# Kernel optimization log

Hardware: AMD Instinct MI355X
Metric: run time of the kernel (lower is better)

Reference implementation:

```python
import jax, jax.numpy as jnp
import numpy as np

N, S, D = 2, 2048, 512
HEADS, HEAD_DIM = 8, 64
SCALE_BASE = 512.0
EPS = 1e-08


def xpos_apply(x, positions, downscale):
    # x: (B, S, d)  positions: (B, S) float
    d = x.shape[-1]
    half = jnp.arange(0, d, 2, dtype=jnp.float32)
    scale_vec = (half + 0.4 * d) / (1.4 * d)                      # (d/2,)
    power = positions[..., None] / SCALE_BASE                     # (B, S, 1)
    scale = scale_vec ** power                                    # (B, S, d/2)
    inv_freq = 1.0 / (10000.0 ** (half / d))                      # (d/2,)
    sinusoid = positions[..., None] * inv_freq                    # (B, S, d/2)
    sin = jnp.sin(sinusoid)
    cos = jnp.cos(sinusoid)
    if downscale:
        scale = 1.0 / scale
    # duplicate-interleave to full dim
    sin = jnp.repeat(sin, 2, axis=-1)
    cos = jnp.repeat(cos, 2, axis=-1)
    scale = jnp.repeat(scale, 2, axis=-1)
    x1 = x[..., 0::2]
    x2 = x[..., 1::2]
    rot = jnp.stack([-x2, x1], axis=-1).reshape(x.shape)          # rotate_every_two
    return (x * cos + rot * sin) * scale


def split_heads(x):
    # (N, S, H*Hd) -> (N*H, S, Hd)
    return x.reshape(N, S, HEADS, HEAD_DIM).transpose(0, 2, 1, 3).reshape(N * HEADS, S, HEAD_DIM)


def setup_inputs() -> dict:
    key = jax.random.key(0)
    ks = jax.random.split(key, 8)
    g = 1.0 / np.sqrt(D)
    return {
        'sequence': jax.random.normal(ks[0], (N, S, D), dtype=jnp.float32),
        'input_mask': jnp.ones((N, S), dtype=jnp.float32),
        'positions': jnp.tile(jnp.arange(S, dtype=jnp.int32), (N, 1)),
        'layer_num': 0,
        'Wq': jax.random.normal(ks[1], (D, D), dtype=jnp.float32) * g,
        'bq': jnp.zeros((D,), dtype=jnp.float32),
        'Wk': jax.random.normal(ks[2], (D, D), dtype=jnp.float32) * g,
        'bk': jnp.zeros((D,), dtype=jnp.float32),
        'Wv': jax.random.normal(ks[3], (D, D), dtype=jnp.float32) * g,
        'bv': jnp.zeros((D,), dtype=jnp.float32),
        'Wo': jax.random.normal(ks[4], (D, D), dtype=jnp.float32) * g,
        'bo': jnp.zeros((D,), dtype=jnp.float32),
    }


def reference(sequence, input_mask, positions, layer_num, Wq, bq, Wk, bk, Wv, bv, Wo, bo):
    scaling = HEAD_DIM ** (-0.5)
    posf = positions.astype(jnp.float32)

    Q = split_heads(sequence @ Wq.T + bq) * scaling               # (N*H, S, Hd)
    K = split_heads(sequence @ Wk.T + bk)
    V = split_heads(sequence @ Wv.T + bv)

    pos_h = jnp.repeat(posf, HEADS, axis=0)                       # 'n s -> (n h) s'
    K = xpos_apply(K, pos_h, downscale=True)
    Q = xpos_apply(Q, pos_h, downscale=False)

    A = jnp.einsum('nsd,ntd->nst', Q, K).reshape(N, HEADS, S, S)  # (N, H, S, S2)
    Vh = V.reshape(N, HEADS, S, HEAD_DIM)

    # causal mask: input_mask over kv dim, lower-triangular
    tri = jnp.tril(jnp.ones((S, S), dtype=jnp.float32))
    attn_mask = input_mask[:, None, None, :] * tri[None, None]    # (N, 1, S, S2)

    A = jax.nn.sigmoid(A) * attn_mask

    # stick-breaking decay: reverse-cumprod of (1 - A) along kv dim, shifted
    Af = jnp.flip(A, axis=(2, 3))
    C = jnp.exp(jnp.cumsum(jnp.log(1.0 - Af + EPS), axis=-1))
    C = jnp.flip(C, axis=(2, 3))
    C = jnp.concatenate([jnp.ones((N, HEADS, S, 1), dtype=C.dtype), C[..., :-1]], axis=-1)

    A = C * A
    attended = jnp.einsum('nhst,nhtd->nhsd', A, Vh)               # (N, H, S, Hd)
    attended = attended.transpose(0, 2, 1, 3).reshape(N, S, HEADS * HEAD_DIM)
    out = attended @ Wo.T + bo
    return out
```

## Files before the change

kernel.cpp:

```cpp
#include <hip/hip_runtime.h>
#include <math.h>

#define S_LEN 2048
#define DMODEL 512
#define HDIM 64
#define EPS_G 1e-8f

typedef __bf16 bf16x8 __attribute__((ext_vector_type(8)));
typedef __bf16 bf16x4 __attribute__((ext_vector_type(4)));
typedef float f32x4 __attribute__((ext_vector_type(4)));

template <int CTRL>
__device__ __forceinline__ float dpp_mov(float src, float oldv) {
  return __int_as_float(__builtin_amdgcn_update_dpp(
      __float_as_int(oldv), __float_as_int(src), CTRL, 0xF, 0xF, false));
}
#define ROW_SHL(n) (0x100 + (n))
#define ROW_SHR(n) (0x110 + (n))

__device__ __forceinline__ float swz_head(float v) {
  return __int_as_float(__builtin_amdgcn_ds_swizzle(__float_as_int(v), 0x0010));
}
__device__ __forceinline__ float swz_tail(float v) {
  return __int_as_float(__builtin_amdgcn_ds_swizzle(__float_as_int(v), 0x01F0));
}

__global__ __launch_bounds__(256) void cvt_kernel(
    const float* __restrict__ X, const float* __restrict__ Wq,
    const float* __restrict__ Wk, const float* __restrict__ Wv,
    const float* __restrict__ Wo,
    __bf16* __restrict__ Xb, __bf16* __restrict__ Wb, __bf16* __restrict__ Wob) {
  const int u = blockIdx.x * 256 + threadIdx.x;
  const float* src; __bf16* dst; int off;
  if (u < 524288)      { src = X;  dst = Xb;          off = u; }
  else if (u < 589824) { src = Wq; dst = Wb;          off = u - 524288; }
  else if (u < 655360) { src = Wk; dst = Wb + 262144; off = u - 589824; }
  else if (u < 720896) { src = Wv; dst = Wb + 524288; off = u - 655360; }
  else                 { src = Wo; dst = Wob;         off = u - 720896; }
  const float4 v = *(const float4*)(src + (size_t)off * 4);
  bf16x4 o;
  o[0] = (__bf16)v.x; o[1] = (__bf16)v.y; o[2] = (__bf16)v.z; o[3] = (__bf16)v.w;
  *(bf16x4*)(dst + (size_t)off * 4) = o;
}

__global__ __launch_bounds__(256, 2) void qkv_gemm(
    const __bf16* __restrict__ Xb, const __bf16* __restrict__ Wb,
    const float* __restrict__ bq, const float* __restrict__ bk, const float* __restrict__ bv,
    const int* __restrict__ pos,
    __bf16* __restrict__ Qh, __bf16* __restrict__ Kh, __bf16* __restrict__ Vt) {
  const int i0 = blockIdx.x << 6;
  const int h  = blockIdx.y;
  const int j0 = h << 6;

  __shared__ __bf16 Xs[64][72];
  __shared__ __bf16 Wls[3][64][72];

  const int tid = threadIdx.x;
  const int wv = tid >> 6, lane = tid & 63;
  const int l = lane & 15, seg = lane >> 4;
  const int sr = tid >> 2, sc = (tid & 3) << 4;

  f32x4 O[3][4];
#pragma unroll
  for (int w = 0; w < 3; ++w)
#pragma unroll
    for (int nt = 0; nt < 4; ++nt) O[w][nt] = (f32x4){0.f, 0.f, 0.f, 0.f};

  bf16x8 xr0, xr1, wr[3][2];
#define LOADQKV(K0)                                                                   \
  {                                                                                   \
    const __bf16* xp = Xb + (size_t)(i0 + sr) * 512 + (K0) + sc;                      \
    xr0 = *(const bf16x8*)xp; xr1 = *(const bf16x8*)(xp + 8);                         \
    _Pragma("unroll")                                                                 \
    for (int w = 0; w < 3; ++w) {                                                     \
      const __bf16* wp = Wb + (size_t)w * 262144 + (size_t)(j0 + sr) * 512 + (K0) + sc;\
      wr[w][0] = *(const bf16x8*)wp; wr[w][1] = *(const bf16x8*)(wp + 8);             \
    }                                                                                 \
  }

  LOADQKV(0)
  for (int k0 = 0; k0 < 512; k0 += 64) {
    __syncthreads();
    *(bf16x8*)&Xs[sr][sc]     = xr0;
    *(bf16x8*)&Xs[sr][sc + 8] = xr1;
#pragma unroll
    for (int w = 0; w < 3; ++w) {
      *(bf16x8*)&Wls[w][sr][sc]     = wr[w][0];
      *(bf16x8*)&Wls[w][sr][sc + 8] = wr[w][1];
    }
    __syncthreads();
    if (k0 < 448) LOADQKV(k0 + 64)

    bf16x8 a0 = *(const bf16x8*)&Xs[wv * 16 + l][seg * 8];
    bf16x8 a1 = *(const bf16x8*)&Xs[wv * 16 + l][seg * 8 + 32];
#pragma unroll
    for (int w = 0; w < 3; ++w)
#pragma unroll
      for (int nt = 0; nt < 4; ++nt) {
        bf16x8 b0 = *(const bf16x8*)&Wls[w][nt * 16 + l][seg * 8];
        bf16x8 b1 = *(const bf16x8*)&Wls[w][nt * 16 + l][seg * 8 + 32];
        O[w][nt] = __builtin_amdgcn_mfma_f32_16x16x32_bf16(a0, b0, O[w][nt], 0, 0, 0);
        O[w][nt] = __builtin_amdgcn_mfma_f32_16x16x32_bf16(a1, b1, O[w][nt], 0, 0, 0);
      }
  }

  const float* const bsrc[3] = {bq, bk, bv};
#pragma unroll
  for (int w = 0; w < 3; ++w)
#pragma unroll
    for (int nt = 0; nt < 4; ++nt) {
      const float bb = bsrc[w][j0 + nt * 16 + l];
#pragma unroll
      for (int reg = 0; reg < 4; ++reg) O[w][nt][reg] += bb;
    }

  const int n = i0 >> 11, sb = i0 & 2047;
  const int nh = (n << 3) + h;
  const int sl = wv * 16 + seg * 4;

  float invf[4], l2sv[4];
#pragma unroll
  for (int nt = 0; nt < 4; ++nt) {
    const float kp = (float)((nt * 16 + l) >> 1);
    invf[nt] = exp2f(-0.41524100f * kp);
    l2sv[nt] = log2f((2.f * kp + 25.6f) * (1.f / 89.6f));
  }
  float pv_[4];
#pragma unroll
  for (int reg = 0; reg < 4; ++reg)
    pv_[reg] = (float)pos[n * S_LEN + sb + sl + reg];

  __syncthreads();

#pragma unroll
  for (int w = 0; w < 2; ++w) {
    const float qs  = (w == 0) ? 0.125f : 1.f;
    const float sgn = (w == 0) ? 1.f : -1.f;
    __bf16* __restrict__ Ob = (w == 0) ? Qh : Kh;
#pragma unroll
    for (int reg = 0; reg < 4; ++reg) {
      const float p = pv_[reg];
#pragma unroll
      for (int nt = 0; nt < 4; ++nt) {
        const float x  = O[w][nt][reg];
        const float xp = __shfl_xor(x, 1);
        const float ang = p * invf[nt];
        const float sn = sinf(ang), cn = cosf(ang);
        const float scl = exp2f(sgn * p * (1.f / 512.f) * l2sv[nt]) * qs;
        const int d = nt * 16 + l;
        const float o = (d & 1) ? (x * cn + xp * sn) : (x * cn - xp * sn);
        Xs[sl + reg][d] = (__bf16)(o * scl);
      }
    }
    __syncthreads();
    __bf16* dst = Ob + (((size_t)nh * S_LEN + sb + sr) << 6) + sc;
    *(bf16x8*)dst       = *(bf16x8*)&Xs[sr][sc];
    *(bf16x8*)(dst + 8) = *(bf16x8*)&Xs[sr][sc + 8];
    __syncthreads();
  }

#pragma unroll
  for (int reg = 0; reg < 4; ++reg)
#pragma unroll
    for (int nt = 0; nt < 4; ++nt)
      Xs[sl + reg][nt * 16 + l] = (__bf16)O[2][nt][reg];
  __syncthreads();
  const int d = tid >> 2, part = tid & 3;
  __bf16 tmp[16];
#pragma unroll
  for (int i = 0; i < 16; ++i) tmp[i] = Xs[part * 16 + i][d];
  __bf16* dst = Vt + (((size_t)(nh * 64 + d)) << 11) + sb + part * 16;
  *(bf16x8*)dst       = *(bf16x8*)&tmp[0];
  *(bf16x8*)(dst + 8) = *(bf16x8*)&tmp[8];
}

__global__ __launch_bounds__(256, 2) void attn_chunk(
    const __bf16* __restrict__ Qh, const __bf16* __restrict__ Kh,
    const __bf16* __restrict__ Vt, const float* __restrict__ imask,
    __bf16* __restrict__ att, float* __restrict__ PartO,
    float* __restrict__ PartP, float* __restrict__ PartA0) {
  const int id = blockIdx.x;
  const int nh = id & 15;
  const int t  = id >> 4;
  int rb, c, nc;
  if (t < 8)       { rb = t; c = 0; nc = 1; }
  else if (t < 24) { int u = t - 8;  rb = 8  + (u >> 1); c = u & 1;     nc = 2; }
  else if (t < 48) { int u = t - 24; rb = 16 + u / 3;    c = u - 3 * (u / 3); nc = 3; }
  else             { int u = t - 48; rb = 24 + (u >> 2); c = u & 3;     nc = 4; }
  const int hi = rb - (c << 3);
  const int lo = (c == nc - 1) ? 0 : hi - 7;

  const int n = nh >> 3, h = nh & 7;
  const int tid = threadIdx.x;
  const int wv = tid >> 6, lane = tid & 63;
  const int l = lane & 15, seg = lane >> 4;
  const int pr = tid >> 3, pc = (tid & 7) << 3;

  __shared__ __bf16 Qs16[64][72];
  __shared__ __bf16 Ks16[64][72];
  __shared__ __bf16 Vt16[64][72];
  __shared__ __bf16 cs16[64][72];
  __shared__ float msk[64];

  for (int idx = tid; idx < 512; idx += 256) {
    int r = idx >> 3, c8 = (idx & 7) << 3;
    *(bf16x8*)&Qs16[r][c8] =
        *(const bf16x8*)(Qh + (((size_t)nh * S_LEN + rb * 64 + r) << 6) + c8);
  }

  f32x4 O[4];
  float pend[4][4];
  float Crow[4];
  float a0k0[4];
#pragma unroll
  for (int nt = 0; nt < 4; ++nt) O[nt] = (f32x4){0.f, 0.f, 0.f, 0.f};
#pragma unroll
  for (int r = 0; r < 4; ++r) {
    Crow[r] = 1.f; a0k0[r] = 0.f;
#pragma unroll
    for (int nt = 0; nt < 4; ++nt) pend[r][nt] = 0.f;
  }

  bf16x8 kp0, kp1, vp0, vp1;
  float mp = 0.f;
#define LOADKV(JT)                                                                     \
  kp0 = *(const bf16x8*)(Kh + (((size_t)nh * S_LEN + (JT) * 64 + pr) << 6) + pc);      \
  kp1 = *(const bf16x8*)(Kh + (((size_t)nh * S_LEN + (JT) * 64 + 32 + pr) << 6) + pc); \
  vp0 = *(const bf16x8*)(Vt + (((size_t)(nh * 64 + pr)) << 11) + (JT) * 64 + pc);      \
  vp1 = *(const bf16x8*)(Vt + (((size_t)(nh * 64 + 32 + pr)) << 11) + (JT) * 64 + pc); \
  if (tid < 64) mp = imask[n * S_LEN + (JT) * 64 + tid];

  LOADKV(hi)

  for (int jt = hi; jt >= lo; --jt) {
    __syncthreads();
    *(bf16x8*)&Ks16[pr][pc]      = kp0;
    *(bf16x8*)&Ks16[32 + pr][pc] = kp1;
    *(bf16x8*)&Vt16[pr][pc]      = vp0;
    *(bf16x8*)&Vt16[32 + pr][pc] = vp1;
    if (tid < 64) msk[tid] = mp;
    __syncthreads();
    if (jt > lo) { LOADKV(jt - 1) }

    bf16x8 aq0 = *(const bf16x8*)&Qs16[wv * 16 + l][seg * 8];
    bf16x8 aq1 = *(const bf16x8*)&Qs16[wv * 16 + l][seg * 8 + 32];
    f32x4 Sv[4];
#pragma unroll
    for (int nt = 0; nt < 4; ++nt) {
      bf16x8 bk0 = *(const bf16x8*)&Ks16[nt * 16 + l][seg * 8];
      bf16x8 bk1 = *(const bf16x8*)&Ks16[nt * 16 + l][seg * 8 + 32];
      f32x4 z = (f32x4){0.f, 0.f, 0.f, 0.f};
      z = __builtin_amdgcn_mfma_f32_16x16x32_bf16(aq0, bk0, z, 0, 0, 0);
      z = __builtin_amdgcn_mfma_f32_16x16x32_bf16(aq1, bk1, z, 0, 0, 0);
      Sv[nt] = z;
    }

    float v0f[4];
#pragma unroll
    for (int nt = 0; nt < 4; ++nt) v0f[nt] = (float)Vt16[nt * 16 + l][0];

#pragma unroll
    for (int reg = 0; reg < 4; ++reg) {
      const int qrow = rb * 64 + wv * 16 + seg * 4 + reg;
      float a_[4], f_[4], p_[4];
#pragma unroll
      for (int nt = 0; nt < 4; ++nt) {
        const int key = jt * 64 + nt * 16 + l;
        const float s = Sv[nt][reg];
        const float mv = msk[nt * 16 + l];
        const float av = (key <= qrow)
            ? mv * __builtin_amdgcn_rcpf(1.f + __expf(-s))
            : 0.f;
        a_[nt] = av;
        f_[nt] = 1.f - av + EPS_G;
      }
#pragma unroll
      for (int nt = 0; nt < 4; ++nt) {
        float p = f_[nt];
        p *= dpp_mov<ROW_SHL(1)>(p, 1.f);
        p *= dpp_mov<ROW_SHL(2)>(p, 1.f);
        p *= dpp_mov<ROW_SHL(4)>(p, 1.f);
        p *= dpp_mov<ROW_SHL(8)>(p, 1.f);
        p_[nt] = p;
      }
      float P_[4], tl[4];
#pragma unroll
      for (int nt = 0; nt < 4; ++nt) {
        P_[nt] = swz_head(p_[nt]);
        tl[nt] = swz_tail(f_[nt]);
      }
      const float a0 = swz_head(a_[0]);
      const float T3 = 1.f, T2 = P_[3], T1 = T2 * P_[2], T0 = T1 * P_[1];
      const float Tarr[4] = {T0, T1, T2, T3};
      const float Ptile = T0 * P_[0];
      const float crow = Crow[reg];
#pragma unroll
      for (int nt = 0; nt < 4; ++nt) {
        const float pprev = dpp_mov<ROW_SHR(1)>(p_[nt], 0.f);
        float cv;
        if (l > 0)
          cv = a_[nt] * pprev * Tarr[nt] * crow;
        else if (nt > 0)
          cv = a_[nt] * tl[nt - 1] * P_[nt] * Tarr[nt] * crow;
        else
          cv = (jt == 0 && nc == 1) ? a_[0] : 0.f;
        cs16[wv * 16 + seg * 4 + reg][nt * 16 + l] = (__bf16)cv;
      }
      if (jt == 0) a0k0[reg] = a0;
      const float f63 = tl[3];
      const float s0  = a0 * Ptile * crow;
      Crow[reg] = crow * Ptile;
#pragma unroll
      for (int nt = 0; nt < 4; ++nt) {
        O[nt][reg] += pend[reg][nt] * f63;
        pend[reg][nt] = s0 * v0f[nt];
      }
    }

    bf16x8 ac0 = *(const bf16x8*)&cs16[wv * 16 + l][seg * 8];
    bf16x8 ac1 = *(const bf16x8*)&cs16[wv * 16 + l][seg * 8 + 32];
#pragma unroll
    for (int nt = 0; nt < 4; ++nt) {
      bf16x8 bv0 = *(const bf16x8*)&Vt16[nt * 16 + l][seg * 8];
      bf16x8 bv1 = *(const bf16x8*)&Vt16[nt * 16 + l][seg * 8 + 32];
      O[nt] = __builtin_amdgcn_mfma_f32_16x16x32_bf16(ac0, bv0, O[nt], 0, 0, 0);
      O[nt] = __builtin_amdgcn_mfma_f32_16x16x32_bf16(ac1, bv1, O[nt], 0, 0, 0);
    }
  }

  if (lo > 0) {
    const int m = lo << 6;
    const float mb = imask[n * S_LEN + m - 1];
    const __bf16* kb = Kh + (((size_t)nh * S_LEN + m - 1) << 6) + seg * 16;
    bf16x8 kb0 = *(const bf16x8*)kb, kb1 = *(const bf16x8*)(kb + 8);
    bf16x8 q0 = *(const bf16x8*)&Qs16[wv * 16 + l][seg * 16];
    bf16x8 q1 = *(const bf16x8*)&Qs16[wv * 16 + l][seg * 16 + 8];
    float sc_ = 0.f;
#pragma unroll
    for (int j = 0; j < 8; ++j)
      sc_ += (float)q0[j] * (float)kb0[j] + (float)q1[j] * (float)kb1[j];
    sc_ += __shfl_xor(sc_, 16);
    sc_ += __shfl_xor(sc_, 32);
    const float fbl = 1.f - mb * __builtin_amdgcn_rcpf(1.f + __expf(-sc_)) + EPS_G;
#pragma unroll
    for (int reg = 0; reg < 4; ++reg) {
      const float fb = __shfl(fbl, (wv << 6 & 0) + (seg << 2) + reg);
#pragma unroll
      for (int nt = 0; nt < 4; ++nt) O[nt][reg] += pend[reg][nt] * fb;
    }
  }

  if (nc == 1) {
#pragma unroll
    for (int nt = 0; nt < 4; ++nt)
#pragma unroll
      for (int reg = 0; reg < 4; ++reg) {
        const int srow = rb * 64 + wv * 16 + seg * 4 + reg;
        att[((size_t)(n * S_LEN + srow)) * DMODEL + h * HDIM + nt * 16 + l] =
            (__bf16)O[nt][reg];
      }
  } else {
    const int slot = nh * 72 + (t - 8);
    float* po = PartO + (size_t)slot * 4096;
#pragma unroll
    for (int nt = 0; nt < 4; ++nt)
#pragma unroll
      for (int reg = 0; reg < 4; ++reg)
        po[(wv * 16 + seg * 4 + reg) * 64 + nt * 16 + l] = O[nt][reg];
    if (l == 0) {
#pragma unroll
      for (int reg = 0; reg < 4; ++reg)
        PartP[slot * 64 + wv * 16 + seg * 4 + reg] = Crow[reg];
      if (lo == 0) {
#pragma unroll
        for (int reg = 0; reg < 4; ++reg)
          PartA0[(nh * 24 + rb - 8) * 64 + wv * 16 + seg * 4 + reg] = a0k0[reg];
      }
    }
  }
}

__global__ __launch_bounds__(256) void combine_kernel(
    const float* __restrict__ PartO, const float* __restrict__ PartP,
    const float* __restrict__ PartA0, const __bf16* __restrict__ Vt,
    __bf16* __restrict__ att) {
  const int b = blockIdx.x;
  const int nh = b / 24;
  const int rb = 8 + (b - nh * 24);
  const int nc = (rb < 16) ? 2 : ((rb < 24) ? 3 : 4);
  const int t0 = (rb < 16) ? 8 + ((rb - 8) << 1)
               : (rb < 24) ? 24 + (rb - 16) * 3
                           : 48 + ((rb - 24) << 2);
  const int n = nh >> 3, h = nh & 7;
  const int tid = threadIdx.x;
  const int r = tid >> 2, db = (tid & 3) << 4;

  float acc[16];
#pragma unroll
  for (int j = 0; j < 16; ++j) acc[j] = 0.f;
  float fac = 1.f;
  for (int c = 0; c < nc; ++c) {
    const int slot = nh * 72 + (t0 - 8) + c;
    const float* po = PartO + (size_t)slot * 4096 + r * 64 + db;
    const float P = PartP[slot * 64 + r];
#pragma unroll
    for (int q = 0; q < 4; ++q) {
      const float4 v = *(const float4*)(po + q * 4);
      acc[q * 4 + 0] += fac * v.x; acc[q * 4 + 1] += fac * v.y;
      acc[q * 4 + 2] += fac * v.z; acc[q * 4 + 3] += fac * v.w;
    }
    fac *= P;
  }
  const float a0 = PartA0[(nh * 24 + rb - 8) * 64 + r];
#pragma unroll
  for (int j = 0; j < 16; ++j)
    acc[j] += a0 * (float)Vt[(((size_t)(nh * 64 + db + j)) << 11)];

  __bf16 ob[16];
#pragma unroll
  for (int j = 0; j < 16; ++j) ob[j] = (__bf16)acc[j];
  __bf16* dst = att + ((size_t)(n * S_LEN + rb * 64 + r)) * DMODEL + h * HDIM + db;
  *(bf16x8*)dst       = *(bf16x8*)&ob[0];
  *(bf16x8*)(dst + 8) = *(bf16x8*)&ob[8];
}

__global__ __launch_bounds__(256, 2) void out_gemm(const __bf16* __restrict__ Xa,
                                                   const __bf16* __restrict__ Wob,
                                                   const float* __restrict__ bo,
                                                   float* __restrict__ Out) {
  const int i0 = blockIdx.x << 6, j0 = blockIdx.y << 7;
  __shared__ __bf16 As[64][72];
  __shared__ __bf16 Bs[128][72];

  const int tid = threadIdx.x;
  const int wv = tid >> 6, lane = tid & 63;
  const int l = lane & 15, seg = lane >> 4;
  const int sr = tid >> 2, sc = (tid & 3) << 4;

  f32x4 O[8];
#pragma unroll
  for (int nt = 0; nt < 8; ++nt) O[nt] = (f32x4){0.f, 0.f, 0.f, 0.f};

  bf16x8 ar0, ar1, br[2][2];
#define LOADOUT(K0)                                                          \
  {                                                                          \
    const __bf16* xp = Xa + (size_t)(i0 + sr) * 512 + (K0) + sc;             \
    ar0 = *(const bf16x8*)xp; ar1 = *(const bf16x8*)(xp + 8);                \
    _Pragma("unroll")                                                        \
    for (int ps = 0; ps < 2; ++ps) {                                         \
      const __bf16* wp = Wob + (size_t)(j0 + ps * 64 + sr) * 512 + (K0) + sc;\
      br[ps][0] = *(const bf16x8*)wp; br[ps][1] = *(const bf16x8*)(wp + 8);  \
    }                                                                        \
  }

  LOADOUT(0)
  for (int k0 = 0; k0 < 512; k0 += 64) {
    __syncthreads();
    *(bf16x8*)&As[sr][sc]     = ar0;
    *(bf16x8*)&As[sr][sc + 8] = ar1;
#pragma unroll
    for (int ps = 0; ps < 2; ++ps) {
      *(bf16x8*)&Bs[ps * 64 + sr][sc]     = br[ps][0];
      *(bf16x8*)&Bs[ps * 64 + sr][sc + 8] = br[ps][1];
    }
    __syncthreads();
    if (k0 < 448) LOADOUT(k0 + 64)

    bf16x8 a0 = *(const bf16x8*)&As[wv * 16 + l][seg * 8];
    bf16x8 a1 = *(const bf16x8*)&As[wv * 16 + l][seg * 8 + 32];
#pragma unroll
    for (int nt = 0; nt < 8; ++nt) {
      bf16x8 b0 = *(const bf16x8*)&Bs[nt * 16 + l][seg * 8];
      bf16x8 b1 = *(const bf16x8*)&Bs[nt * 16 + l][seg * 8 + 32];
      O[nt] = __builtin_amdgcn_mfma_f32_16x16x32_bf16(a0, b0, O[nt], 0, 0, 0);
      O[nt] = __builtin_amdgcn_mfma_f32_16x16x32_bf16(a1, b1, O[nt], 0, 0, 0);
    }
  }

#pragma unroll
  for (int nt = 0; nt < 8; ++nt) {
    const float bb = bo[j0 + nt * 16 + l];
#pragma unroll
    for (int reg = 0; reg < 4; ++reg) {
      const int m = wv * 16 + seg * 4 + reg;
      Out[(size_t)(i0 + m) * 512 + j0 + nt * 16 + l] = O[nt][reg] + bb;
    }
  }
}

extern "C" void kernel_launch(void* const* d_in, const int* in_sizes, int n_in,
                              void* d_out, int out_size, void* d_ws, size_t ws_size,
                              hipStream_t stream) {
  (void)in_sizes; (void)n_in; (void)out_size; (void)ws_size;
  const float* seq  = (const float*)d_in[0];
  const float* mask = (const float*)d_in[1];
  const int*   pos  = (const int*)d_in[2];
  const float* Wq = (const float*)d_in[4];
  const float* bq = (const float*)d_in[5];
  const float* Wk = (const float*)d_in[6];
  const float* bk = (const float*)d_in[7];
  const float* Wv = (const float*)d_in[8];
  const float* bv = (const float*)d_in[9];
  const float* Wo = (const float*)d_in[10];
  const float* bo = (const float*)d_in[11];
  float* out = (float*)d_out;

  char* base = (char*)d_ws;
  __bf16* att = (__bf16*)base;
  __bf16* Qh  = (__bf16*)(base + ( 4u << 20));
  __bf16* Kh  = (__bf16*)(base + ( 8u << 20));
  __bf16* Vt  = (__bf16*)(base + (12u << 20));
  __bf16* Wb  = (__bf16*)(base + (16u << 20));
  __bf16* Wob = (__bf16*)(base + (18u << 20));
  __bf16* Xb  = (__bf16*)(base + (19u << 20));
  float* PartO  = (float*)(base + (23u << 20));
  float* PartP  = (float*)(base + (42u << 20));
  float* PartA0 = (float*)(base + (43u << 20));

  cvt_kernel<<<3072, 256, 0, stream>>>(seq, Wq, Wk, Wv, Wo, Xb, Wb, Wob);
  qkv_gemm<<<dim3(64, 8), 256, 0, stream>>>(Xb, Wb, bq, bk, bv, pos, Qh, Kh, Vt);
  attn_chunk<<<1280, 256, 0, stream>>>(Qh, Kh, Vt, mask, att, PartO, PartP, PartA0);
  combine_kernel<<<384, 256, 0, stream>>>(PartO, PartP, PartA0, Vt, att);
  out_gemm<<<dim3(64, 4), 256, 0, stream>>>(att, Wob, bo, out);
}
```

Measured before the change: 174.6 us.

## Use 128-row query tiles with 512-thread attention blocks and fuse xpos epilogue

The attention chunk kernel now handles 128 query rows per block with 8 waves, so each K/V tile loaded into shared memory serves twice as many queries. Block count halves, scheduling is reversed so heavy blocks launch first, and the combine kernel is remapped to match. The QKV epilogue computes sin/cos and scale once per element for both Q and K using hardware sin/cos on a revolution-normalized angle and a reciprocal, then writes Q, K and V after a single barrier. The risks are lower occupancy and coarser load balance from the larger blocks, plus precision changes from the hardware trig and reciprocal.

```diff
diff --git a/kernel.cpp b/kernel.cpp
--- a/kernel.cpp
+++ b/kernel.cpp
@@ -122,7 +122,7 @@
 #pragma unroll
   for (int nt = 0; nt < 4; ++nt) {
     const float kp = (float)((nt * 16 + l) >> 1);
-    invf[nt] = exp2f(-0.41524100f * kp);
+    invf[nt] = exp2f(-0.41524100f * kp) * 0.15915494f;
     l2sv[nt] = log2f((2.f * kp + 25.6f) * (1.f / 89.6f));
   }
   float pv_[4];
@@ -133,61 +133,62 @@
   __syncthreads();
 
 #pragma unroll
-  for (int w = 0; w < 2; ++w) {
-    const float qs  = (w == 0) ? 0.125f : 1.f;
-    const float sgn = (w == 0) ? 1.f : -1.f;
-    __bf16* __restrict__ Ob = (w == 0) ? Qh : Kh;
-#pragma unroll
-    for (int reg = 0; reg < 4; ++reg) {
-      const float p = pv_[reg];
-#pragma unroll
-      for (int nt = 0; nt < 4; ++nt) {
-        const float x  = O[w][nt][reg];
-        const float xp = __shfl_xor(x, 1);
-        const float ang = p * invf[nt];
-        const float sn = sinf(ang), cn = cosf(ang);
-        const float scl = exp2f(sgn * p * (1.f / 512.f) * l2sv[nt]) * qs;
-        const int d = nt * 16 + l;
-        const float o = (d & 1) ? (x * cn + xp * sn) : (x * cn - xp * sn);
-        Xs[sl + reg][d] = (__bf16)(o * scl);
-      }
-    }
-    __syncthreads();
-    __bf16* dst = Ob + (((size_t)nh * S_LEN + sb + sr) << 6) + sc;
-    *(bf16x8*)dst       = *(bf16x8*)&Xs[sr][sc];
-    *(bf16x8*)(dst + 8) = *(bf16x8*)&Xs[sr][sc + 8];
-    __syncthreads();
-  }
-
-#pragma unroll
-  for (int reg = 0; reg < 4; ++reg)
-#pragma unroll
-    for (int nt = 0; nt < 4; ++nt)
-      Xs[sl + reg][nt * 16 + l] = (__bf16)O[2][nt][reg];
+  for (int reg = 0; reg < 4; ++reg) {
+    const float p = pv_[reg];
+#pragma unroll
+    for (int nt = 0; nt < 4; ++nt) {
+      const int d = nt * 16 + l;
+      const float rev0 = p * invf[nt];
+      const float rev  = rev0 - floorf(rev0);
+      const float sn = __builtin_amdgcn_sinf(rev);
+      const float cn = __builtin_amdgcn_cosf(rev);
+      const float e  = p * (1.f / 512.f) * l2sv[nt];
+      const float sq = exp2f(e);
+      const float sQ = sq * 0.125f;
+      const float sK = __builtin_amdgcn_rcpf(sq);
+      float x  = O[0][nt][reg];
+      float xp = __shfl_xor(x, 1);
+      Xs[sl + reg][d] =
+          (__bf16)((((d & 1) ? (x * cn + xp * sn) : (x * cn - xp * sn))) * sQ);
+      x  = O[1][nt][reg];
+      xp = __shfl_xor(x, 1);
+      Wls[0][sl + reg][d] =
+          (__bf16)((((d & 1) ? (x * cn + xp * sn) : (x * cn - xp * sn))) * sK);
+      Wls[1][sl + reg][d] = (__bf16)O[2][nt][reg];
+    }
+  }
   __syncthreads();
+
+  __bf16* qdst = Qh + (((size_t)nh * S_LEN + sb + sr) << 6) + sc;
+  *(bf16x8*)qdst       = *(bf16x8*)&Xs[sr][sc];
+  *(bf16x8*)(qdst + 8) = *(bf16x8*)&Xs[sr][sc + 8];
+  __bf16* kdst = Kh + (((size_t)nh * S_LEN + sb + sr) << 6) + sc;
+  *(bf16x8*)kdst       = *(bf16x8*)&Wls[0][sr][sc];
+  *(bf16x8*)(kdst + 8) = *(bf16x8*)&Wls[0][sr][sc + 8];
+
   const int d = tid >> 2, part = tid & 3;
   __bf16 tmp[16];
 #pragma unroll
-  for (int i = 0; i < 16; ++i) tmp[i] = Xs[part * 16 + i][d];
-  __bf16* dst = Vt + (((size_t)(nh * 64 + d)) << 11) + sb + part * 16;
-  *(bf16x8*)dst       = *(bf16x8*)&tmp[0];
-  *(bf16x8*)(dst + 8) = *(bf16x8*)&tmp[8];
-}
-
-__global__ __launch_bounds__(256, 2) void attn_chunk(
+  for (int i = 0; i < 16; ++i) tmp[i] = Wls[1][part * 16 + i][d];
+  __bf16* vdst = Vt + (((size_t)(nh * 64 + d)) << 11) + sb + part * 16;
+  *(bf16x8*)vdst       = *(bf16x8*)&tmp[0];
+  *(bf16x8*)(vdst + 8) = *(bf16x8*)&tmp[8];
+}
+
+__global__ __launch_bounds__(512, 4) void attn_chunk(
     const __bf16* __restrict__ Qh, const __bf16* __restrict__ Kh,
     const __bf16* __restrict__ Vt, const float* __restrict__ imask,
     __bf16* __restrict__ att, float* __restrict__ PartO,
     float* __restrict__ PartP, float* __restrict__ PartA0) {
-  const int id = blockIdx.x;
+  const int id = 639 - blockIdx.x;
   const int nh = id & 15;
   const int t  = id >> 4;
-  int rb, c, nc;
-  if (t < 8)       { rb = t; c = 0; nc = 1; }
-  else if (t < 24) { int u = t - 8;  rb = 8  + (u >> 1); c = u & 1;     nc = 2; }
-  else if (t < 48) { int u = t - 24; rb = 16 + u / 3;    c = u - 3 * (u / 3); nc = 3; }
-  else             { int u = t - 48; rb = 24 + (u >> 2); c = u & 3;     nc = 4; }
-  const int hi = rb - (c << 3);
+  int rb2, c, nc;
+  if (t < 4)       { rb2 = t; c = 0; nc = 1; }
+  else if (t < 12) { int u = t - 4;  rb2 = 4  + (u >> 1); c = u & 1; nc = 2; }
+  else if (t < 24) { int u = t - 12; rb2 = 8  + u / 3;    c = u - 3 * (u / 3); nc = 3; }
+  else             { int u = t - 24; rb2 = 12 + (u >> 2); c = u & 3; nc = 4; }
+  const int hi = 2 * rb2 + 1 - (c << 3);
   const int lo = (c == nc - 1) ? 0 : hi - 7;
 
   const int n = nh >> 3, h = nh & 7;
@@ -196,16 +197,16 @@
   const int l = lane & 15, seg = lane >> 4;
   const int pr = tid >> 3, pc = (tid & 7) << 3;
 
-  __shared__ __bf16 Qs16[64][72];
+  __shared__ __bf16 Qs16[128][72];
   __shared__ __bf16 Ks16[64][72];
   __shared__ __bf16 Vt16[64][72];
-  __shared__ __bf16 cs16[64][72];
+  __shared__ __bf16 cs16[128][72];
   __shared__ float msk[64];
 
-  for (int idx = tid; idx < 512; idx += 256) {
+  for (int idx = tid; idx < 1024; idx += 512) {
     int r = idx >> 3, c8 = (idx & 7) << 3;
     *(bf16x8*)&Qs16[r][c8] =
-        *(const bf16x8*)(Qh + (((size_t)nh * S_LEN + rb * 64 + r) << 6) + c8);
+        *(const bf16x8*)(Qh + (((size_t)nh * S_LEN + rb2 * 128 + r) << 6) + c8);
   }
 
   f32x4 O[4];
@@ -221,23 +222,19 @@
     for (int nt = 0; nt < 4; ++nt) pend[r][nt] = 0.f;
   }
 
-  bf16x8 kp0, kp1, vp0, vp1;
+  bf16x8 kp0, vp0;
   float mp = 0.f;
-#define LOADKV(JT)                                                                     \
-  kp0 = *(const bf16x8*)(Kh + (((size_t)nh * S_LEN + (JT) * 64 + pr) << 6) + pc);      \
-  kp1 = *(const bf16x8*)(Kh + (((size_t)nh * S_LEN + (JT) * 64 + 32 + pr) << 6) + pc); \
-  vp0 = *(const bf16x8*)(Vt + (((size_t)(nh * 64 + pr)) << 11) + (JT) * 64 + pc);      \
-  vp1 = *(const bf16x8*)(Vt + (((size_t)(nh * 64 + 32 + pr)) << 11) + (JT) * 64 + pc); \
+#define LOADKV(JT)                                                                  \
+  kp0 = *(const bf16x8*)(Kh + (((size_t)nh * S_LEN + (JT) * 64 + pr) << 6) + pc);   \
+  vp0 = *(const bf16x8*)(Vt + (((size_t)(nh * 64 + pr)) << 11) + (JT) * 64 + pc);   \
   if (tid < 64) mp = imask[n * S_LEN + (JT) * 64 + tid];
 
   LOADKV(hi)
 
   for (int jt = hi; jt >= lo; --jt) {
     __syncthreads();
-    *(bf16x8*)&Ks16[pr][pc]      = kp0;
-    *(bf16x8*)&Ks16[32 + pr][pc] = kp1;
-    *(bf16x8*)&Vt16[pr][pc]      = vp0;
-    *(bf16x8*)&Vt16[32 + pr][pc] = vp1;
+    *(bf16x8*)&Ks16[pr][pc] = kp0;
+    *(bf16x8*)&Vt16[pr][pc] = vp0;
     if (tid < 64) msk[tid] = mp;
     __syncthreads();
     if (jt > lo) { LOADKV(jt - 1) }
@@ -261,7 +258,7 @@
 
 #pragma unroll
     for (int reg = 0; reg < 4; ++reg) {
-      const int qrow = rb * 64 + wv * 16 + seg * 4 + reg;
+      const int qrow = rb2 * 128 + wv * 16 + seg * 4 + reg;
       float a_[4], f_[4], p_[4];
 #pragma unroll
       for (int nt = 0; nt < 4; ++nt) {
@@ -344,7 +341,7 @@
     const float fbl = 1.f - mb * __builtin_amdgcn_rcpf(1.f + __expf(-sc_)) + EPS_G;
 #pragma unroll
     for (int reg = 0; reg < 4; ++reg) {
-      const float fb = __shfl(fbl, (wv << 6 & 0) + (seg << 2) + reg);
+      const float fb = __shfl(fbl, (seg << 2) + reg);
 #pragma unroll
       for (int nt = 0; nt < 4; ++nt) O[nt][reg] += pend[reg][nt] * fb;
     }
@@ -355,13 +352,13 @@
     for (int nt = 0; nt < 4; ++nt)
 #pragma unroll
       for (int reg = 0; reg < 4; ++reg) {
-        const int srow = rb * 64 + wv * 16 + seg * 4 + reg;
+        const int srow = rb2 * 128 + wv * 16 + seg * 4 + reg;
         att[((size_t)(n * S_LEN + srow)) * DMODEL + h * HDIM + nt * 16 + l] =
             (__bf16)O[nt][reg];
       }
   } else {
-    const int slot = nh * 72 + (t - 8);
-    float* po = PartO + (size_t)slot * 4096;
+    const int slot = nh * 36 + (t - 4);
+    float* po = PartO + (size_t)slot * 8192;
 #pragma unroll
     for (int nt = 0; nt < 4; ++nt)
 #pragma unroll
@@ -370,11 +367,11 @@
     if (l == 0) {
 #pragma unroll
       for (int reg = 0; reg < 4; ++reg)
-        PartP[slot * 64 + wv * 16 + seg * 4 + reg] = Crow[reg];
+        PartP[slot * 128 + wv * 16 + seg * 4 + reg] = Crow[reg];
       if (lo == 0) {
 #pragma unroll
         for (int reg = 0; reg < 4; ++reg)
-          PartA0[(nh * 24 + rb - 8) * 64 + wv * 16 + seg * 4 + reg] = a0k0[reg];
+          PartA0[(nh * 12 + rb2 - 4) * 128 + wv * 16 + seg * 4 + reg] = a0k0[reg];
       }
     }
   }
@@ -385,43 +382,45 @@
     const float* __restrict__ PartA0, const __bf16* __restrict__ Vt,
     __bf16* __restrict__ att) {
   const int b = blockIdx.x;
-  const int nh = b / 24;
-  const int rb = 8 + (b - nh * 24);
-  const int nc = (rb < 16) ? 2 : ((rb < 24) ? 3 : 4);
-  const int t0 = (rb < 16) ? 8 + ((rb - 8) << 1)
-               : (rb < 24) ? 24 + (rb - 16) * 3
-                           : 48 + ((rb - 24) << 2);
+  const int nh = b / 12;
+  const int rb2 = 4 + (b - nh * 12);
+  const int nc = (rb2 < 8) ? 2 : ((rb2 < 12) ? 3 : 4);
+  const int t0 = (rb2 < 8) ? 4 + ((rb2 - 4) << 1)
+               : (rb2 < 12) ? 12 + (rb2 - 8) * 3
+                            : 24 + ((rb2 - 12) << 2);
   const int n = nh >> 3, h = nh & 7;
   const int tid = threadIdx.x;
-  const int r = tid >> 2, db = (tid & 3) << 4;
-
-  float acc[16];
-#pragma unroll
-  for (int j = 0; j < 16; ++j) acc[j] = 0.f;
+  const int r = tid >> 1, db = (tid & 1) << 5;
+
+  float acc[32];
+#pragma unroll
+  for (int j = 0; j < 32; ++j) acc[j] = 0.f;
   float fac = 1.f;
   for (int c = 0; c < nc; ++c) {
-    const int slot = nh * 72 + (t0 - 8) + c;
-    const float* po = PartO + (size_t)slot * 4096 + r * 64 + db;
-    const float P = PartP[slot * 64 + r];
-#pragma unroll
-    for (int q = 0; q < 4; ++q) {
+    const int slot = nh * 36 + (t0 - 4) + c;
+    const float* po = PartO + (size_t)slot * 8192 + r * 64 + db;
+    const float P = PartP[slot * 128 + r];
+#pragma unroll
+    for (int q = 0; q < 8; ++q) {
       const float4 v = *(const float4*)(po + q * 4);
       acc[q * 4 + 0] += fac * v.x; acc[q * 4 + 1] += fac * v.y;
       acc[q * 4 + 2] += fac * v.z; acc[q * 4 + 3] += fac * v.w;
     }
     fac *= P;
   }
-  const float a0 = PartA0[(nh * 24 + rb - 8) * 64 + r];
-#pragma unroll
-  for (int j = 0; j < 16; ++j)
+  const float a0 = PartA0[(nh * 12 + rb2 - 4) * 128 + r];
+#pragma unroll
+  for (int j = 0; j < 32; ++j)
     acc[j] += a0 * (float)Vt[(((size_t)(nh * 64 + db + j)) << 11)];
 
-  __bf16 ob[16];
-#pragma unroll
-  for (int j = 0; j < 16; ++j) ob[j] = (__bf16)acc[j];
-  __bf16* dst = att + ((size_t)(n * S_LEN + rb * 64 + r)) * DMODEL + h * HDIM + db;
-  *(bf16x8*)dst       = *(bf16x8*)&ob[0];
-  *(bf16x8*)(dst + 8) = *(bf16x8*)&ob[8];
+  __bf16 ob[32];
+#pragma unroll
+  for (int j = 0; j < 32; ++j) ob[j] = (__bf16)acc[j];
+  __bf16* dst = att + ((size_t)(n * S_LEN + rb2 * 128 + r)) * DMODEL + h * HDIM + db;
+  *(bf16x8*)dst        = *(bf16x8*)&ob[0];
+  *(bf16x8*)(dst + 8)  = *(bf16x8*)&ob[8];
+  *(bf16x8*)(dst + 16) = *(bf16x8*)&ob[16];
+  *(bf16x8*)(dst + 24) = *(bf16x8*)&ob[24];
 }
 
 __global__ __launch_bounds__(256, 2) void out_gemm(const __bf16* __restrict__ Xa,
@@ -519,7 +518,7 @@
 
   cvt_kernel<<<3072, 256, 0, stream>>>(seq, Wq, Wk, Wv, Wo, Xb, Wb, Wob);
   qkv_gemm<<<dim3(64, 8), 256, 0, stream>>>(Xb, Wb, bq, bk, bv, pos, Qh, Kh, Vt);
-  attn_chunk<<<1280, 256, 0, stream>>>(Qh, Kh, Vt, mask, att, PartO, PartP, PartA0);
-  combine_kernel<<<384, 256, 0, stream>>>(PartO, PartP, PartA0, Vt, att);
+  attn_chunk<<<640, 512, 0, stream>>>(Qh, Kh, Vt, mask, att, PartO, PartP, PartA0);
+  combine_kernel<<<192, 256, 0, stream>>>(PartO, PartP, PartA0, Vt, att);
   out_gemm<<<dim3(64, 4), 256, 0, stream>>>(att, Wob, bo, out);
 }
```

Result: no change. 176.4 us (+1.0%).

## Reassign GEMM warp tiles by output column and hoist xPos trig per column

Applied to the files above, without the earlier changes.

In the QKV and output projection kernels, each wave now owns a 16-column slice of the output across all 64 rows instead of a 16-row slice across all columns. As a result, the per-column xPos frequency, scale and bias are computed once per thread instead of once per column tile. The rotary path uses hardware sin/cos on a range-reduced revolution count and a reciprocal for the K downscale, so one exp2 serves both Q and K. Q, K and V are staged into separate shared buffers with a single barrier instead of three sequential store phases, which cuts barriers and transcendental work at some cost to trig precision.

```diff
diff --git a/kernel.cpp b/kernel.cpp
--- a/kernel.cpp
+++ b/kernel.cpp
@@ -64,7 +64,7 @@
 #pragma unroll
   for (int w = 0; w < 3; ++w)
 #pragma unroll
-    for (int nt = 0; nt < 4; ++nt) O[w][nt] = (f32x4){0.f, 0.f, 0.f, 0.f};
+    for (int r4 = 0; r4 < 4; ++r4) O[w][r4] = (f32x4){0.f, 0.f, 0.f, 0.f};
 
   bf16x8 xr0, xr1, wr[3][2];
 #define LOADQKV(K0)                                                                   \
@@ -91,87 +91,85 @@
     __syncthreads();
     if (k0 < 448) LOADQKV(k0 + 64)
 
-    bf16x8 a0 = *(const bf16x8*)&Xs[wv * 16 + l][seg * 8];
-    bf16x8 a1 = *(const bf16x8*)&Xs[wv * 16 + l][seg * 8 + 32];
-#pragma unroll
-    for (int w = 0; w < 3; ++w)
-#pragma unroll
-      for (int nt = 0; nt < 4; ++nt) {
-        bf16x8 b0 = *(const bf16x8*)&Wls[w][nt * 16 + l][seg * 8];
-        bf16x8 b1 = *(const bf16x8*)&Wls[w][nt * 16 + l][seg * 8 + 32];
-        O[w][nt] = __builtin_amdgcn_mfma_f32_16x16x32_bf16(a0, b0, O[w][nt], 0, 0, 0);
-        O[w][nt] = __builtin_amdgcn_mfma_f32_16x16x32_bf16(a1, b1, O[w][nt], 0, 0, 0);
-      }
-  }
-
-  const float* const bsrc[3] = {bq, bk, bv};
-#pragma unroll
-  for (int w = 0; w < 3; ++w)
-#pragma unroll
-    for (int nt = 0; nt < 4; ++nt) {
-      const float bb = bsrc[w][j0 + nt * 16 + l];
-#pragma unroll
-      for (int reg = 0; reg < 4; ++reg) O[w][nt][reg] += bb;
+    bf16x8 a0[4], a1[4];
+#pragma unroll
+    for (int r4 = 0; r4 < 4; ++r4) {
+      a0[r4] = *(const bf16x8*)&Xs[r4 * 16 + l][seg * 8];
+      a1[r4] = *(const bf16x8*)&Xs[r4 * 16 + l][seg * 8 + 32];
+    }
+#pragma unroll
+    for (int w = 0; w < 3; ++w) {
+      bf16x8 b0 = *(const bf16x8*)&Wls[w][wv * 16 + l][seg * 8];
+      bf16x8 b1 = *(const bf16x8*)&Wls[w][wv * 16 + l][seg * 8 + 32];
+#pragma unroll
+      for (int r4 = 0; r4 < 4; ++r4) {
+        O[w][r4] = __builtin_amdgcn_mfma_f32_16x16x32_bf16(a0[r4], b0, O[w][r4], 0, 0, 0);
+        O[w][r4] = __builtin_amdgcn_mfma_f32_16x16x32_bf16(a1[r4], b1, O[w][r4], 0, 0, 0);
+      }
+    }
+  }
+
+  const int d = wv * 16 + l;
+  const float bbq = bq[j0 + d], bbk = bk[j0 + d], bbv = bv[j0 + d];
+#pragma unroll
+  for (int r4 = 0; r4 < 4; ++r4)
+#pragma unroll
+    for (int reg = 0; reg < 4; ++reg) {
+      O[0][r4][reg] += bbq; O[1][r4][reg] += bbk; O[2][r4][reg] += bbv;
     }
 
   const int n = i0 >> 11, sb = i0 & 2047;
   const int nh = (n << 3) + h;
-  const int sl = wv * 16 + seg * 4;
-
-  float invf[4], l2sv[4];
-#pragma unroll
-  for (int nt = 0; nt < 4; ++nt) {
-    const float kp = (float)((nt * 16 + l) >> 1);
-    invf[nt] = exp2f(-0.41524100f * kp);
-    l2sv[nt] = log2f((2.f * kp + 25.6f) * (1.f / 89.6f));
-  }
-  float pv_[4];
-#pragma unroll
-  for (int reg = 0; reg < 4; ++reg)
-    pv_[reg] = (float)pos[n * S_LEN + sb + sl + reg];
+
+  const float kp   = (float)(d >> 1);
+  const float invf = exp2f(-0.41524100f * kp) * 0.15915494f;
+  const float l2sv = log2f((2.f * kp + 25.6f) * (1.f / 89.6f));
+  float pv_[4][4];
+#pragma unroll
+  for (int r4 = 0; r4 < 4; ++r4)
+#pragma unroll
+    for (int reg = 0; reg < 4; ++reg)
+      pv_[r4][reg] = (float)pos[n * S_LEN + sb + r4 * 16 + (seg << 2) + reg];
 
   __syncthreads();
 
 #pragma unroll
-  for (int w = 0; w < 2; ++w) {
-    const float qs  = (w == 0) ? 0.125f : 1.f;
-    const float sgn = (w == 0) ? 1.f : -1.f;
-    __bf16* __restrict__ Ob = (w == 0) ? Qh : Kh;
+  for (int r4 = 0; r4 < 4; ++r4)
 #pragma unroll
     for (int reg = 0; reg < 4; ++reg) {
-      const float p = pv_[reg];
-#pragma unroll
-      for (int nt = 0; nt < 4; ++nt) {
-        const float x  = O[w][nt][reg];
-        const float xp = __shfl_xor(x, 1);
-        const float ang = p * invf[nt];
-        const float sn = sinf(ang), cn = cosf(ang);
-        const float scl = exp2f(sgn * p * (1.f / 512.f) * l2sv[nt]) * qs;
-        const int d = nt * 16 + l;
-        const float o = (d & 1) ? (x * cn + xp * sn) : (x * cn - xp * sn);
-        Xs[sl + reg][d] = (__bf16)(o * scl);
-      }
-    }
-    __syncthreads();
-    __bf16* dst = Ob + (((size_t)nh * S_LEN + sb + sr) << 6) + sc;
-    *(bf16x8*)dst       = *(bf16x8*)&Xs[sr][sc];
-    *(bf16x8*)(dst + 8) = *(bf16x8*)&Xs[sr][sc + 8];
-    __syncthreads();
-  }
-
-#pragma unroll
-  for (int reg = 0; reg < 4; ++reg)
-#pragma unroll
-    for (int nt = 0; nt < 4; ++nt)
-      Xs[sl + reg][nt * 16 + l] = (__bf16)O[2][nt][reg];
+      const int row = r4 * 16 + (seg << 2) + reg;
+      const float p = pv_[r4][reg];
+      const float rev0 = p * invf;
+      const float rev  = rev0 - floorf(rev0);
+      const float sn = __builtin_amdgcn_sinf(rev);
+      const float cn = __builtin_amdgcn_cosf(rev);
+      const float sq = exp2f(p * (1.f / 512.f) * l2sv);
+      const float sQ = sq * 0.125f;
+      const float sK = __builtin_amdgcn_rcpf(sq);
+      float x  = O[0][r4][reg];
+      float xp = __shfl_xor(x, 1);
+      Xs[row][d] = (__bf16)((((d & 1) ? (x * cn + xp * sn) : (x * cn - xp * sn))) * sQ);
+      x  = O[1][r4][reg];
+      xp = __shfl_xor(x, 1);
+      Wls[0][row][d] = (__bf16)((((d & 1) ? (x * cn + xp * sn) : (x * cn - xp * sn))) * sK);
+      Wls[1][row][d] = (__bf16)O[2][r4][reg];
+    }
   __syncthreads();
-  const int d = tid >> 2, part = tid & 3;
+
+  __bf16* qdst = Qh + (((size_t)nh * S_LEN + sb + sr) << 6) + sc;
+  *(bf16x8*)qdst       = *(bf16x8*)&Xs[sr][sc];
+  *(bf16x8*)(qdst + 8) = *(bf16x8*)&Xs[sr][sc + 8];
+  __bf16* kdst = Kh + (((size_t)nh * S_LEN + sb + sr) << 6) + sc;
+  *(bf16x8*)kdst       = *(bf16x8*)&Wls[0][sr][sc];
+  *(bf16x8*)(kdst + 8) = *(bf16x8*)&Wls[0][sr][sc + 8];
+
+  const int dv = tid >> 2, part = tid & 3;
   __bf16 tmp[16];
 #pragma unroll
-  for (int i = 0; i < 16; ++i) tmp[i] = Xs[part * 16 + i][d];
-  __bf16* dst = Vt + (((size_t)(nh * 64 + d)) << 11) + sb + part * 16;
-  *(bf16x8*)dst       = *(bf16x8*)&tmp[0];
-  *(bf16x8*)(dst + 8) = *(bf16x8*)&tmp[8];
+  for (int i = 0; i < 16; ++i) tmp[i] = Wls[1][part * 16 + i][dv];
+  __bf16* vdst = Vt + (((size_t)(nh * 64 + dv)) << 11) + sb + part * 16;
+  *(bf16x8*)vdst       = *(bf16x8*)&tmp[0];
+  *(bf16x8*)(vdst + 8) = *(bf16x8*)&tmp[8];
 }
 
 __global__ __launch_bounds__(256, 2) void attn_chunk(
@@ -344,7 +342,7 @@
     const float fbl = 1.f - mb * __builtin_amdgcn_rcpf(1.f + __expf(-sc_)) + EPS_G;
 #pragma unroll
     for (int reg = 0; reg < 4; ++reg) {
-      const float fb = __shfl(fbl, (wv << 6 & 0) + (seg << 2) + reg);
+      const float fb = __shfl(fbl, (seg << 2) + reg);
 #pragma unroll
       for (int nt = 0; nt < 4; ++nt) O[nt][reg] += pend[reg][nt] * fb;
     }
@@ -437,9 +435,11 @@
   const int l = lane & 15, seg = lane >> 4;
   const int sr = tid >> 2, sc = (tid & 3) << 4;
 
-  f32x4 O[8];
-#pragma unroll
-  for (int nt = 0; nt < 8; ++nt) O[nt] = (f32x4){0.f, 0.f, 0.f, 0.f};
+  f32x4 O[2][4];
+#pragma unroll
+  for (int j = 0; j < 2; ++j)
+#pragma unroll
+    for (int r4 = 0; r4 < 4; ++r4) O[j][r4] = (f32x4){0.f, 0.f, 0.f, 0.f};
 
   bf16x8 ar0, ar1, br[2][2];
 #define LOADOUT(K0)                                                          \
@@ -466,25 +466,36 @@
     __syncthreads();
     if (k0 < 448) LOADOUT(k0 + 64)
 
-    bf16x8 a0 = *(const bf16x8*)&As[wv * 16 + l][seg * 8];
-    bf16x8 a1 = *(const bf16x8*)&As[wv * 16 + l][seg * 8 + 32];
-#pragma unroll
-    for (int nt = 0; nt < 8; ++nt) {
-      bf16x8 b0 = *(const bf16x8*)&Bs[nt * 16 + l][seg * 8];
-      bf16x8 b1 = *(const bf16x8*)&Bs[nt * 16 + l][seg * 8 + 32];
-      O[nt] = __builtin_amdgcn_mfma_f32_16x16x32_bf16(a0, b0, O[nt], 0, 0, 0);
-      O[nt] = __builtin_amdgcn_mfma_f32_16x16x32_bf16(a1, b1, O[nt], 0, 0, 0);
-    }
-  }
-
-#pragma unroll
-  for (int nt = 0; nt < 8; ++nt) {
-    const float bb = bo[j0 + nt * 16 + l];
-#pragma unroll
-    for (int reg = 0; reg < 4; ++reg) {
-      const int m = wv * 16 + seg * 4 + reg;
-      Out[(size_t)(i0 + m) * 512 + j0 + nt * 16 + l] = O[nt][reg] + bb;
-    }
+    bf16x8 a0[4], a1[4];
+#pragma unroll
+    for (int r4 = 0; r4 < 4; ++r4) {
+      a0[r4] = *(const bf16x8*)&As[r4 * 16 + l][seg * 8];
+      a1[r4] = *(const bf16x8*)&As[r4 * 16 + l][seg * 8 + 32];
+    }
+#pragma unroll
+    for (int j = 0; j < 2; ++j) {
+      const int u = wv + 4 * j;
+      bf16x8 b0 = *(const bf16x8*)&Bs[u * 16 + l][seg * 8];
+      bf16x8 b1 = *(const bf16x8*)&Bs[u * 16 + l][seg * 8 + 32];
+#pragma unroll
+      for (int r4 = 0; r4 < 4; ++r4) {
+        O[j][r4] = __builtin_amdgcn_mfma_f32_16x16x32_bf16(a0[r4], b0, O[j][r4], 0, 0, 0);
+        O[j][r4] = __builtin_amdgcn_mfma_f32_16x16x32_bf16(a1[r4], b1, O[j][r4], 0, 0, 0);
+      }
+    }
+  }
+
+#pragma unroll
+  for (int j = 0; j < 2; ++j) {
+    const int u = wv + 4 * j;
+    const float bb = bo[j0 + u * 16 + l];
+#pragma unroll
+    for (int r4 = 0; r4 < 4; ++r4)
+#pragma unroll
+      for (int reg = 0; reg < 4; ++reg) {
+        const int m = r4 * 16 + (seg << 2) + reg;
+        Out[(size_t)(i0 + m) * 512 + j0 + u * 16 + l] = O[j][r4][reg] + bb;
+      }
   }
 }
 
```

Result: faster. 167.1 us (-4.3%).
